# Performance work log

Measured on AMD Instinct MI355X. Metric: run time of the kernel, lower is better.

The kernel has to match this reference:

```python
import jax, jax.numpy as jnp
import numpy as np

B, N, CZ, CH, CA, H, TN = 1, 256, 128, 128, 32, 4, 4


def setup_inputs() -> dict:
    key = jax.random.key(0)
    ks = iter(jax.random.split(key, 64))

    def rn(shape, s=0.02):
        return jax.random.normal(next(ks), shape, dtype=jnp.float32) * s

    d = {"z": jax.random.normal(next(ks), (B, N, N, CZ), dtype=jnp.float32)}
    # Triangle multiplication params, stacked [2, ...]: idx 0 = outgoing, 1 = incoming
    d["tm_ln_in_w"] = jnp.ones((2, CZ)); d["tm_ln_in_b"] = jnp.zeros((2, CZ))
    for nm, shp in [("ap", (2, CZ, CH)), ("ag", (2, CZ, CH)), ("bp", (2, CZ, CH)),
                    ("bg", (2, CZ, CH)), ("g", (2, CZ, CZ)), ("zo", (2, CH, CZ))]:
        d[f"tm_{nm}_w"] = rn(shp)
        d[f"tm_{nm}_b"] = jnp.zeros((2, shp[-1]))
    d["tm_lnout_w"] = jnp.ones((2, CH)); d["tm_lnout_b"] = jnp.zeros((2, CH))
    # Triangle attention params, stacked [2, ...]: idx 0 = start, 1 = end
    d["ta_ln_w"] = jnp.ones((2, CZ)); d["ta_ln_b"] = jnp.zeros((2, CZ))
    d["ta_q_w"] = rn((2, CZ, H * CA)); d["ta_k_w"] = rn((2, CZ, H * CA)); d["ta_v_w"] = rn((2, CZ, H * CA))
    d["ta_b_w"] = rn((2, CZ, H))
    d["ta_g_w"] = rn((2, CZ, H * CA)); d["ta_g_b"] = jnp.zeros((2, H * CA))
    d["ta_o_w"] = rn((2, H * CA, CZ)); d["ta_o_b"] = jnp.zeros((2, CZ))
    # Pair transition
    d["pt_ln_w"] = jnp.ones((CZ,)); d["pt_ln_b"] = jnp.zeros((CZ,))
    d["pt_1_w"] = rn((CZ, TN * CZ)); d["pt_1_b"] = jnp.zeros((TN * CZ,))
    d["pt_2_w"] = rn((TN * CZ, CZ)); d["pt_2_b"] = jnp.zeros((CZ,))
    return d


def _ln(x, w, b, eps=1e-5):
    m = jnp.mean(x, axis=-1, keepdims=True)
    v = jnp.mean(jnp.square(x - m), axis=-1, keepdims=True)
    return (x - m) * jax.lax.rsqrt(v + eps) * w + b


def _tri_mul(z, lnw, lnb, apw, apb, agw, agb, bpw, bpb, bgw, bgb, gw, gb,
             lnow, lnob, zw, zb, outgoing):
    x = _ln(z, lnw, lnb)
    a = jax.nn.sigmoid(x @ agw + agb) * (x @ apw + apb)  # [B,I,J,CH]
    b = jax.nn.sigmoid(x @ bgw + bgb) * (x @ bpw + bpb)
    eq = 'bikc,bjkc->bijc' if outgoing else 'bkic,bkjc->bijc'
    t = jnp.einsum(eq, a, b)  # O(N^3 * CH)
    t = _ln(t, lnow, lnob) @ zw + zb
    return t * jax.nn.sigmoid(x @ gw + gb)


def _tri_att(z, lnw, lnb, qw, kw, vw, bw, gw, gb, ow, ob):
    Bz, I, J, _ = z.shape
    x = _ln(z, lnw, lnb)
    # triangle bias [B,1,H,I,J] (broadcast over query row)
    bias = jnp.einsum('bijc,ch->bhij', x, bw)[:, None]
    q = (x @ qw).reshape(Bz, I, J, H, CA).transpose(0, 1, 3, 2, 4) / np.float32(np.sqrt(CA))
    k = (x @ kw).reshape(Bz, I, J, H, CA).transpose(0, 1, 3, 2, 4)
    v = (x @ vw).reshape(Bz, I, J, H, CA).transpose(0, 1, 3, 2, 4)
    a = jnp.einsum('bihqc,bihkc->bihqk', q, k) + bias  # [B,I,H,J,J]
    p = jax.nn.softmax(a, axis=-1)
    o = jnp.einsum('bihqk,bihkc->bihqc', p, v).transpose(0, 1, 3, 2, 4).reshape(Bz, I, J, H * CA)
    o = o * jax.nn.sigmoid(x @ gw + gb)
    return o @ ow + ob


def reference(z, tm_ln_in_w, tm_ln_in_b, tm_ap_w, tm_ap_b, tm_ag_w, tm_ag_b,
              tm_bp_w, tm_bp_b, tm_bg_w, tm_bg_b, tm_g_w, tm_g_b,
              tm_lnout_w, tm_lnout_b, tm_zo_w, tm_zo_b,
              ta_ln_w, ta_ln_b, ta_q_w, ta_k_w, ta_v_w, ta_b_w,
              ta_g_w, ta_g_b, ta_o_w, ta_o_b,
              pt_ln_w, pt_ln_b, pt_1_w, pt_1_b, pt_2_w, pt_2_b):
    def tm(zz, i, outgoing):
        return _tri_mul(zz, tm_ln_in_w[i], tm_ln_in_b[i], tm_ap_w[i], tm_ap_b[i],
                        tm_ag_w[i], tm_ag_b[i], tm_bp_w[i], tm_bp_b[i],
                        tm_bg_w[i], tm_bg_b[i], tm_g_w[i], tm_g_b[i],
                        tm_lnout_w[i], tm_lnout_b[i], tm_zo_w[i], tm_zo_b[i], outgoing)

    def ta(zz, i):
        return _tri_att(zz, ta_ln_w[i], ta_ln_b[i], ta_q_w[i], ta_k_w[i], ta_v_w[i],
                        ta_b_w[i], ta_g_w[i], ta_g_b[i], ta_o_w[i], ta_o_b[i])

    z = z + tm(z, 0, True)          # triangle mult outgoing + residual (dropout = eval identity)
    z = z + tm(z, 1, False)         # triangle mult incoming + residual
    z = z + ta(z, 0)                # triangle attention (starting node)
    zt = jnp.swapaxes(z, 1, 2)      # transpose for ending-node attention
    zt = zt + ta(zt, 1)
    z = jnp.swapaxes(zt, 1, 2)
    x = _ln(z, pt_ln_w, pt_ln_b)    # pair transition
    z = z + (jax.nn.relu(x @ pt_1_w + pt_1_b) @ pt_2_w + pt_2_b)
    return z
```

## Files before the change

kernel.cpp:

```cpp
#include <hip/hip_runtime.h>
#include <math.h>

#define N_  256
#define NN  65536
#define CZ  128
#define CH  128
#define H_  4
#define CA  32

typedef __attribute__((ext_vector_type(8))) short bf16x8;
typedef __attribute__((ext_vector_type(4))) float f32x4;

__device__ __forceinline__ float sigmoidf_(float x){ return 1.f/(1.f+__expf(-x)); }

__device__ __forceinline__ short f2b(float f){
  unsigned u = __float_as_uint(f);
  unsigned r = (u + 0x7fffu + ((u>>16)&1u)) >> 16;
  return (short)r;
}
__device__ __forceinline__ float b2f(short s){
  unsigned u = ((unsigned)(unsigned short)s) << 16;
  return __uint_as_float(u);
}
__device__ __forceinline__ unsigned pk_bf16(float lo, float hi){
  unsigned r;
  asm volatile("v_cvt_pk_bf16_f32 %0, %1, %2" : "=v"(r) : "v"(lo), "v"(hi));
  return r;
}

__device__ __forceinline__ void glds16(const void* g, const void* l){
  __builtin_amdgcn_global_load_lds((const __attribute__((address_space(1))) void*)g,
                                   (__attribute__((address_space(3))) void*)l, 16, 0, 0);
}

__device__ __forceinline__ float wave_red_sum(float v){
  #pragma unroll
  for(int o=32;o>0;o>>=1) v += __shfl_xor(v,o,64);
  return v;
}

__device__ __forceinline__ int Gperm(int t, int m){
  return ((t>>1)<<5) + ((m>>2)<<3) + ((t&1)<<2) + (m&3);
}

__global__ void __launch_bounds__(256) prep_weights(
    const float* tm_ag, const float* tm_ap, const float* tm_bg, const float* tm_bp,
    const float* tm_g, const float* tm_zo,
    const float* ta_q, const float* ta_k, const float* ta_v, const float* ta_g, const float* ta_o,
    const float* pt1, const float* pt2, short* Wf){
  int tid = threadIdx.x;
  int g = blockIdx.x*4 + (tid>>6);
  int l = tid & 63;
  int s = blockIdx.y;
  const float* src; int ldn = 128, koff = 0, noff = 0;
  if (s < 12){
    int i = s/6, w = s - i*6;
    switch(w){ case 0: src=tm_ag; break; case 1: src=tm_ap; break; case 2: src=tm_bg; break;
               case 3: src=tm_bp; break; case 4: src=tm_g;  break; default: src=tm_zo; }
    src += i*16384;
  } else if (s < 22){
    int t2 = s-12; int i = t2/5, w = t2 - i*5;
    switch(w){ case 0: src=ta_q; break; case 1: src=ta_k; break; case 2: src=ta_v; break;
               case 3: src=ta_g; break; default: src=ta_o; }
    src += i*16384;
  } else if (s < 26){
    src = pt1; ldn = 512; noff = (s-22)*128;
  } else {
    src = pt2; koff = (s-26)*128;
  }
  int nt = g>>2, ks = g&3;
  int n = noff + nt*16 + (l&15);
  int kb = koff + ks*32 + (l>>4)*8;
  short tmp[8];
  #pragma unroll
  for (int e=0;e<8;e++) tmp[e] = f2b(src[(size_t)(kb+e)*ldn + n]);
  short* dst = Wf + s*16384 + ((nt*4+ks)*64 + l)*8;
  *(short4*)dst     = *(short4*)&tmp[0];
  *(short4*)(dst+4) = *(short4*)&tmp[4];
}

template<bool TRANS>
__global__ void __launch_bounds__(256) ln_x(const float* __restrict__ in,
                                            const float* __restrict__ w,
                                            const float* __restrict__ b,
                                            short* __restrict__ out){
  int wid  = threadIdx.x >> 6;
  int lane = threadIdx.x & 63;
  int row  = blockIdx.x*4 + wid;
  int irow;
  if (TRANS){ int i = row >> 8, j = row & 255; irow = (j<<8) | i; } else irow = row;
  float v0 = in[(size_t)irow*CZ + lane];
  float v1 = in[(size_t)irow*CZ + lane + 64];
  float m  = wave_red_sum(v0+v1) * (1.f/128.f);
  float d0 = v0-m, d1 = v1-m;
  float var = wave_red_sum(d0*d0 + d1*d1) * (1.f/128.f);
  float r = rsqrtf(var + 1e-5f);
  out[(size_t)row*CZ + lane]      = f2b(d0*r*w[lane]    + b[lane]);
  out[(size_t)row*CZ + lane + 64] = f2b(d1*r*w[lane+64] + b[lane+64]);
}

__device__ __forceinline__ void stage128_8(const short* __restrict__ g, short* xs, int r0, int tid){
  #pragma unroll
  for (int m=0;m<4;++m){
    int d = m*512 + tid;
    int row = d>>4, cw = d&15;
    glds16(&g[(size_t)(r0+row)*128 + ((cw ^ (row&15))<<3)], xs + (size_t)(d & ~63)*8);
  }
}

__device__ __forceinline__ bf16x8 ldsA(const short* xs, int row, int ch){
  return *(const bf16x8*)&xs[row*128 + ((ch ^ (row&15))<<3)];
}

__device__ __forceinline__ void gemm_core8(const short* xs, const short* __restrict__ wf,
                                           int wm, int wn, int l, f32x4 (&acc)[2][4]){
  #pragma unroll
  for (int ks=0; ks<4; ++ks){
    bf16x8 a[2], b[4];
    #pragma unroll
    for (int mt=0; mt<2; ++mt)
      a[mt] = ldsA(xs, wm*32 + mt*16 + (l&15), ks*4 + (l>>4));
    #pragma unroll
    for (int nt=0; nt<4; ++nt)
      b[nt] = *(const bf16x8*)&wf[(((wn*4+nt)*4 + ks)*64 + l)*8];
    #pragma unroll
    for (int mt=0; mt<2; ++mt)
      #pragma unroll
      for (int nt=0; nt<4; ++nt)
        acc[mt][nt] = __builtin_amdgcn_mfma_f32_16x16x32_bf16(a[mt], b[nt], acc[mt][nt], 0,0,0);
  }
}

__device__ __forceinline__ void gemm_core28(const short* xs, const short* __restrict__ wf1,
                                            const short* __restrict__ wf2,
                                            int wm, int wn, int l,
                                            f32x4 (&acc1)[2][4], f32x4 (&acc2)[2][4]){
  #pragma unroll
  for (int ks=0; ks<4; ++ks){
    bf16x8 a[2], b1[4], b2[4];
    #pragma unroll
    for (int mt=0; mt<2; ++mt)
      a[mt] = ldsA(xs, wm*32 + mt*16 + (l&15), ks*4 + (l>>4));
    #pragma unroll
    for (int nt=0; nt<4; ++nt){
      b1[nt] = *(const bf16x8*)&wf1[(((wn*4+nt)*4 + ks)*64 + l)*8];
      b2[nt] = *(const bf16x8*)&wf2[(((wn*4+nt)*4 + ks)*64 + l)*8];
    }
    #pragma unroll
    for (int mt=0; mt<2; ++mt)
      #pragma unroll
      for (int nt=0; nt<4; ++nt){
        acc1[mt][nt] = __builtin_amdgcn_mfma_f32_16x16x32_bf16(a[mt], b1[nt], acc1[mt][nt], 0,0,0);
        acc2[mt][nt] = __builtin_amdgcn_mfma_f32_16x16x32_bf16(a[mt], b2[nt], acc2[mt][nt], 0,0,0);
      }
  }
}

#define ZERO_ACC(A) { _Pragma("unroll") for(int _a=0;_a<2;_a++) _Pragma("unroll") for(int _b=0;_b<4;_b++) A[_a][_b]=(f32x4){0,0,0,0}; }

#define GEMM_PROLOG8 \
  int tid = threadIdx.x; int r0 = blockIdx.x*128; \
  int wid = tid>>6, l = tid&63; int wm = wid>>1, wn = wid&1; (void)r0;

#define EPI8 \
  int row = wm*32 + mt*16 + ((l>>4)<<2) + reg; \
  int col = wn*64 + nt*16 + (l&15);

#define FOR_EPI for (int mt=0;mt<2;++mt) for (int nt=0;nt<4;++nt) for (int reg=0;reg<4;++reg)

__global__ void __launch_bounds__(512) k_quad_gate(const short* __restrict__ X,
                                                   const short* __restrict__ Wagf, const float* __restrict__ bag,
                                                   const short* __restrict__ Wapf, const float* __restrict__ bap,
                                                   const short* __restrict__ Wbgf, const float* __restrict__ bbg,
                                                   const short* __restrict__ Wbpf, const float* __restrict__ bbp,
                                                   short* __restrict__ out1, short* __restrict__ out2){
  __shared__ short xs[128*128];
  GEMM_PROLOG8
  stage128_8(X, xs, r0, tid);
  __syncthreads();
  {
    f32x4 ag[2][4], ap[2][4];
    ZERO_ACC(ag) ZERO_ACC(ap)
    gemm_core28(xs, Wagf, Wapf, wm, wn, l, ag, ap);
    FOR_EPI{
      EPI8
      float v = (ap[mt][nt][reg] + bap[col]) * sigmoidf_(ag[mt][nt][reg] + bag[col]);
      out1[(size_t)(r0+row)*128 + col] = f2b(v);
    }
  }
  {
    f32x4 bg2[2][4], bp2[2][4];
    ZERO_ACC(bg2) ZERO_ACC(bp2)
    gemm_core28(xs, Wbgf, Wbpf, wm, wn, l, bg2, bp2);
    FOR_EPI{
      EPI8
      float v = (bp2[mt][nt][reg] + bbp[col]) * sigmoidf_(bg2[mt][nt][reg] + bbg[col]);
      out2[(size_t)(r0+row)*128 + col] = f2b(v);
    }
  }
}

__global__ void __launch_bounds__(512) k_qkv(const short* __restrict__ X,
                                             const short* __restrict__ Wqf, float sq,
                                             const short* __restrict__ Wkf,
                                             const short* __restrict__ Wvf,
                                             short* __restrict__ out_q, short* __restrict__ out_k,
                                             short* __restrict__ Vt){
  __shared__ short xs[128*128];
  GEMM_PROLOG8
  stage128_8(X, xs, r0, tid);
  __syncthreads();
  {
    f32x4 aq[2][4], ak[2][4];
    ZERO_ACC(aq) ZERO_ACC(ak)
    gemm_core28(xs, Wqf, Wkf, wm, wn, l, aq, ak);
    FOR_EPI{
      EPI8
      out_q[(size_t)(r0+row)*128 + col] = f2b(aq[mt][nt][reg]*sq);
      out_k[(size_t)(r0+row)*128 + col] = f2b(ak[mt][nt][reg]);
    }
  }
  f32x4 av[2][4];
  ZERO_ACC(av)
  gemm_core8(xs, Wvf, wm, wn, l, av);
  __syncthreads();
  #pragma unroll
  for (int mt=0;mt<2;++mt)
    #pragma unroll
    for (int nt=0;nt<4;++nt){
      int rb  = wm*32 + mt*16 + ((l>>4)<<2);
      int col = wn*64 + nt*16 + (l&15);
      short4 s4 = { f2b(av[mt][nt][0]), f2b(av[mt][nt][1]), f2b(av[mt][nt][2]), f2b(av[mt][nt][3]) };
      *(short4*)&xs[col*128 + (((rb>>3) ^ (col&15))<<3) + (rb&7)] = s4;
    }
  __syncthreads();
  int i = r0>>8, j0 = r0&255;
  #pragma unroll
  for (int m=0;m<4;++m){
    int d = m*512 + tid;
    int c = d>>4, ch = d&15;
    int4 val = *(const int4*)&xs[c*128 + ((ch ^ (c&15))<<3)];
    *(int4*)&Vt[(size_t)((i*4 + (c>>5))*32 + (c&31))*256 + j0 + ch*8] = val;
  }
}

__global__ void __launch_bounds__(512) k_tri_finish(const short* __restrict__ Tb,
                                                    const short* __restrict__ X,
                                                    const short* __restrict__ Wzf, const float* __restrict__ bz,
                                                    const short* __restrict__ Wgf, const float* __restrict__ bg,
                                                    const float* __restrict__ lnw, const float* __restrict__ lnb,
                                                    const float* __restrict__ zin, float* __restrict__ zout){
  __shared__ short tt[128*128];
  __shared__ short xs[128*128];
  __shared__ float ps[512], pq[512];
  __shared__ float mu[128], iv[128];
  GEMM_PROLOG8
  stage128_8(X, xs, r0, tid);
  #pragma unroll
  for (int m=0;m<4;++m){
    int d = m*512 + tid;
    int c = d>>4, ch = d&15;
    glds16(&Tb[(size_t)c*65536 + r0 + ch*8], tt + (size_t)(d & ~63)*8);
  }
  __syncthreads();
  int rl = tid & 127, cq = tid >> 7;
  float vals[32]; float s = 0.f, q = 0.f;
  #pragma unroll
  for (int cc=0; cc<32; ++cc){
    float v = b2f(tt[(cq*32+cc)*128 + rl]);
    vals[cc] = v; s += v; q += v*v;
  }
  ps[cq*128 + rl] = s; pq[cq*128 + rl] = q;
  __syncthreads();
  if (tid < 128){
    float ss = ps[tid]+ps[128+tid]+ps[256+tid]+ps[384+tid];
    float qq = pq[tid]+pq[128+tid]+pq[256+tid]+pq[384+tid];
    float m = ss * (1.f/128.f);
    float var = qq * (1.f/128.f) - m*m;
    mu[tid] = m; iv[tid] = rsqrtf(var + 1e-5f);
  }
  __syncthreads();
  {
    float m = mu[rl], r = iv[rl];
    #pragma unroll
    for (int chq=0; chq<4; ++chq){
      short tmp[8];
      #pragma unroll
      for (int e=0;e<8;++e){
        int cc = chq*8 + e;
        int c = cq*32 + cc;
        tmp[e] = f2b((vals[cc]-m)*r*lnw[c] + lnb[c]);
      }
      int ch = cq*4 + chq;
      *(int4*)&tt[rl*128 + ((ch ^ (rl&15))<<3)] = *(int4*)tmp;
    }
  }
  __syncthreads();
  f32x4 az[2][4], ag[2][4];
  ZERO_ACC(az) ZERO_ACC(ag)
  gemm_core8(tt, Wzf, wm, wn, l, az);
  gemm_core8(xs, Wgf, wm, wn, l, ag);
  FOR_EPI{
    EPI8
    size_t idx = (size_t)(r0+row)*128 + col;
    float v = (az[mt][nt][reg] + bz[col]) * sigmoidf_(ag[mt][nt][reg] + bg[col]);
    zout[idx] = zin[idx] + v;
  }
}

template<bool TRANS>
__global__ void __launch_bounds__(512) k_attn_out(const short* __restrict__ O,
                                                  const short* __restrict__ X,
                                                  const short* __restrict__ Wgf, const float* __restrict__ bg,
                                                  const short* __restrict__ Wof, const float* __restrict__ bo,
                                                  float* __restrict__ z){
  __shared__ short xs[128*128];
  __shared__ short os[128*128];
  GEMM_PROLOG8
  stage128_8(X, xs, r0, tid);
  #pragma unroll
  for (int m=0;m<4;++m){
    int d = m*512 + tid;
    int row = d>>4, ch = d&15;
    glds16(&O[(size_t)(r0+row)*128 + ch*8], os + (size_t)(d & ~63)*8);
  }
  __syncthreads();
  f32x4 ag[2][4];
  ZERO_ACC(ag)
  gemm_core8(xs, Wgf, wm, wn, l, ag);
  __syncthreads();
  FOR_EPI{
    EPI8
    float ov = b2f(os[row*128 + col]);
    float v = ov * sigmoidf_(ag[mt][nt][reg] + bg[col]);
    xs[row*128 + (((col>>3) ^ (row&15))<<3) + (col&7)] = f2b(v);
  }
  __syncthreads();
  f32x4 a2[2][4];
  ZERO_ACC(a2)
  gemm_core8(xs, Wof, wm, wn, l, a2);
  FOR_EPI{
    EPI8
    int orow = r0+row;
    int zrow = TRANS ? (((orow&255)<<8) | (orow>>8)) : orow;
    z[(size_t)zrow*128 + col] += a2[mt][nt][reg] + bo[col];
  }
}

__global__ void __launch_bounds__(512) k_pt(const short* __restrict__ X,
                                            const short* __restrict__ W1f, const float* __restrict__ b1,
                                            const short* __restrict__ W2f, const float* __restrict__ b2,
                                            float* __restrict__ z){
  __shared__ short xs[128*128];
  __shared__ short hs[128*128];
  GEMM_PROLOG8
  stage128_8(X, xs, r0, tid);
  __syncthreads();
  f32x4 a2[2][4];
  ZERO_ACC(a2)
  for (int m=0;m<4;++m){
    f32x4 a1[2][4];
    ZERO_ACC(a1)
    gemm_core8(xs, W1f + m*16384, wm, wn, l, a1);
    FOR_EPI{
      EPI8
      float v = fmaxf(a1[mt][nt][reg] + b1[m*128 + col], 0.f);
      hs[row*128 + (((col>>3) ^ (row&15))<<3) + (col&7)] = f2b(v);
    }
    __syncthreads();
    gemm_core8(hs, W2f + m*16384, wm, wn, l, a2);
    __syncthreads();
  }
  FOR_EPI{
    EPI8
    z[(size_t)(r0+row)*128 + col] += a2[mt][nt][reg] + b2[col];
  }
}

template<bool TR>
__global__ void __launch_bounds__(256) pack_cxy(const short* __restrict__ inA, const short* __restrict__ inB,
                                                short* __restrict__ outA, short* __restrict__ outB){
  __shared__ short tile[256*144];
  const short* in = blockIdx.y ? inB : inA;
  short* out      = blockIdx.y ? outB : outA;
  int x = blockIdx.x, tid = threadIdx.x;
  #pragma unroll
  for (int m=0;m<16;++m){
    int idx = m*256 + tid;
    int y = idx>>4, c0 = (idx&15)*8;
    int r = TR ? (y*256 + x) : (x*256 + y);
    *(int4*)&tile[y*144 + c0] = *(const int4*)&in[(size_t)r*128 + c0];
  }
  __syncthreads();
  int c = tid & 127, yh = tid >> 7;
  short* ob = out + (size_t)c*65536 + x*256 + yh*128;
  #pragma unroll
  for (int yc=0; yc<16; ++yc){
    short tmp[8];
    #pragma unroll
    for (int e=0;e<8;e++) tmp[e] = tile[(yh*128 + yc*8 + e)*144 + c];
    *(int4*)&ob[yc*8] = *(int4*)tmp;
  }
}

__global__ void __launch_bounds__(512) k_einsum(const short* __restrict__ Ab,
                                                const short* __restrict__ Bb,
                                                short* __restrict__ Tb){
  __shared__ short as[128*64];
  __shared__ short bs[128*64];
  int c = blockIdx.z;
  int i0 = blockIdx.x*128, j0 = blockIdx.y*128;
  const short* A = Ab + (size_t)c*65536;
  const short* B = Bb + (size_t)c*65536;
  int tid = threadIdx.x;
  int wid = tid>>6, l = tid&63; int wm = wid>>1, wn = wid&1;
  f32x4 acc[2][4];
  ZERO_ACC(acc)
  for (int kt=0; kt<4; ++kt){
    __syncthreads();
    #pragma unroll
    for (int m=0;m<2;++m){
      int d = m*512 + tid;
      int row = d>>3, cw = d&7;
      glds16(&A[(size_t)(i0+row)*256 + kt*64 + ((cw ^ (row&7))<<3)], as + (size_t)(d & ~63)*8);
      glds16(&B[(size_t)(j0+row)*256 + kt*64 + ((cw ^ (row&7))<<3)], bs + (size_t)(d & ~63)*8);
    }
    __syncthreads();
    #pragma unroll
    for (int ks=0; ks<2; ++ks){
      bf16x8 a[2], b[4];
      #pragma unroll
      for (int mt=0; mt<2; ++mt){
        int row = wm*32 + mt*16 + (l&15);
        int ch  = (ks*4 + (l>>4)) ^ (row&7);
        a[mt] = *(const bf16x8*)&as[row*64 + ch*8];
      }
      #pragma unroll
      for (int nt=0; nt<4; ++nt){
        int row = wn*64 + nt*16 + (l&15);
        int ch  = (ks*4 + (l>>4)) ^ (row&7);
        b[nt] = *(const bf16x8*)&bs[row*64 + ch*8];
      }
      #pragma unroll
      for (int mt=0; mt<2; ++mt)
        #pragma unroll
        for (int nt=0; nt<4; ++nt)
          acc[mt][nt] = __builtin_amdgcn_mfma_f32_16x16x32_bf16(a[mt], b[nt], acc[mt][nt], 0,0,0);
    }
  }
  short* To = Tb + (size_t)c*65536;
  FOR_EPI{
    int row = wm*32 + mt*16 + ((l>>4)<<2) + reg;
    int col = wn*64 + nt*16 + (l&15);
    To[(size_t)(i0+row)*256 + j0+col] = f2b(acc[mt][nt][reg]);
  }
}

__global__ void __launch_bounds__(256) bias_gemm(const short* __restrict__ X,
                                                 const float* __restrict__ bw,
                                                 float* __restrict__ BSF){
  __shared__ float xs[64][129];
  int r0 = blockIdx.x*64;
  for(int idx=threadIdx.x; idx<64*128; idx+=256)
    xs[idx>>7][idx&127] = b2f(X[(size_t)(r0+(idx>>7))*CZ + (idx&127)]);
  __syncthreads();
  int h = threadIdx.x>>6, r = threadIdx.x&63;
  float acc=0.f;
  #pragma unroll 4
  for(int k=0;k<CZ;k++) acc += xs[r][k]*bw[k*H_+h];
  int rr2 = r0 + r;
  int q = rr2 >> 8, j = rr2 & 255;
  int t = ((j>>5)<<1) + ((j>>2)&1);
  int m = (((j>>3)&3)<<2) + (j&3);
  int idx = (((h*16 + (q>>4))*16 + t) << 8) + (((m>>2)*16 + (q&15)) << 2) + (m&3);
  BSF[idx] = acc;
}

__global__ void __launch_bounds__(256, 3) attn_mfma(const short* __restrict__ Qg,
                                                    const short* __restrict__ Kg,
                                                    const short* __restrict__ Vt,
                                                    const float* __restrict__ BSF,
                                                    short* __restrict__ O){
  __shared__ short Kf[8192];
  __shared__ short Vf[8192];
  int i = blockIdx.x, h = blockIdx.y;
  int tid = threadIdx.x;
  #pragma unroll
  for (int m=0;m<4;++m){
    int d = m*256 + tid;
    int t = d>>6, ll = d&63;
    glds16(&Kg[(size_t)(i*N_ + Gperm(t, ll&15))*CH + h*CA + ((ll>>4)<<3)],
           Kf + (size_t)(d & ~63)*8);
    glds16(&Vt[(size_t)(((i*H_ + h)*CA) + ((t>>3)<<4) + (ll&15))*N_ + ((t&7)<<5) + ((ll>>4)<<3)],
           Vf + (size_t)(d & ~63)*8);
  }
  __syncthreads();

  int wid = tid >> 6, l = tid & 63;
  int lg = l >> 4, ln = l & 15;

  for (int ss=0; ss<4; ++ss){
    int sub = wid*4 + ss;
    bf16x8 qfrag = *(const bf16x8*)&Qg[(size_t)(i*N_ + sub*16 + ln)*CH + h*CA + (lg<<3)];
    const float* bb = BSF + (size_t)(h*16 + sub)*4096 + (l<<2);
    f32x4 acc[16];
    #pragma unroll
    for (int t=0;t<16;t++) acc[t] = *(const f32x4*)&bb[t<<8];
    #pragma unroll
    for (int t=0;t<16;t++){
      bf16x8 kf = *(const bf16x8*)&Kf[t*512 + l*8];
      acc[t] = __builtin_amdgcn_mfma_f32_16x16x32_bf16(kf, qfrag, acc[t], 0,0,0);
    }
    float mx = -1e30f;
    #pragma unroll
    for (int t=0;t<16;t++)
      mx = fmaxf(mx, fmaxf(fmaxf(acc[t][0],acc[t][1]), fmaxf(acc[t][2],acc[t][3])));
    mx = fmaxf(mx, __shfl_xor(mx,16,64));
    mx = fmaxf(mx, __shfl_xor(mx,32,64));
    float sum = 0.f;
    #pragma unroll
    for (int t=0;t<16;t++){
      #pragma unroll
      for (int r=0;r<4;r++){ float p = __expf(acc[t][r]-mx); acc[t][r]=p; sum += p; }
    }
    sum += __shfl_xor(sum,16,64);
    sum += __shfl_xor(sum,32,64);
    float iv = 1.0f / sum;
    bf16x8 pf[8];
    #pragma unroll
    for (int jt=0;jt<8;jt++){
      int4 w4;
      w4.x = pk_bf16(acc[2*jt  ][0], acc[2*jt  ][1]);
      w4.y = pk_bf16(acc[2*jt  ][2], acc[2*jt  ][3]);
      w4.z = pk_bf16(acc[2*jt+1][0], acc[2*jt+1][1]);
      w4.w = pk_bf16(acc[2*jt+1][2], acc[2*jt+1][3]);
      pf[jt] = *(bf16x8*)&w4;
    }
    #pragma unroll
    for (int ct=0; ct<2; ++ct){
      f32x4 oe = {0.f,0.f,0.f,0.f}, oo = {0.f,0.f,0.f,0.f};
      #pragma unroll
      for (int jt=0;jt<8;jt+=2){
        bf16x8 ve = *(const bf16x8*)&Vf[((ct*8 + jt  )*64 + l)*8];
        bf16x8 vo = *(const bf16x8*)&Vf[((ct*8 + jt+1)*64 + l)*8];
        oe = __builtin_amdgcn_mfma_f32_16x16x32_bf16(ve, pf[jt  ], oe, 0,0,0);
        oo = __builtin_amdgcn_mfma_f32_16x16x32_bf16(vo, pf[jt+1], oo, 0,0,0);
      }
      int q = sub*16 + ln;
      int c = ct*16 + lg*4;
      short4 ov = { f2b((oe[0]+oo[0])*iv), f2b((oe[1]+oo[1])*iv),
                    f2b((oe[2]+oo[2])*iv), f2b((oe[3]+oo[3])*iv) };
      *(short4*)&O[(size_t)(i*N_ + q)*CH + h*CA + c] = ov;
    }
  }
}

extern "C" void kernel_launch(void* const* d_in, const int* in_sizes, int n_in,
                              void* d_out, int out_size, void* d_ws, size_t ws_size,
                              hipStream_t stream) {
  const float* z_in      = (const float*)d_in[0];
  const float* tm_lnin_w = (const float*)d_in[1];
  const float* tm_lnin_b = (const float*)d_in[2];
  const float* tm_ap_w   = (const float*)d_in[3];
  const float* tm_ap_b   = (const float*)d_in[4];
  const float* tm_ag_w   = (const float*)d_in[5];
  const float* tm_ag_b   = (const float*)d_in[6];
  const float* tm_bp_w   = (const float*)d_in[7];
  const float* tm_bp_b   = (const float*)d_in[8];
  const float* tm_bg_w   = (const float*)d_in[9];
  const float* tm_bg_b   = (const float*)d_in[10];
  const float* tm_g_w    = (const float*)d_in[11];
  const float* tm_g_b    = (const float*)d_in[12];
  const float* tm_zo_w   = (const float*)d_in[13];
  const float* tm_zo_b   = (const float*)d_in[14];
  const float* tm_lno_w  = (const float*)d_in[15];
  const float* tm_lno_b  = (const float*)d_in[16];
  const float* ta_ln_w   = (const float*)d_in[17];
  const float* ta_ln_b   = (const float*)d_in[18];
  const float* ta_q_w    = (const float*)d_in[19];
  const float* ta_k_w    = (const float*)d_in[20];
  const float* ta_v_w    = (const float*)d_in[21];
  const float* ta_b_w    = (const float*)d_in[22];
  const float* ta_g_w    = (const float*)d_in[23];
  const float* ta_g_b    = (const float*)d_in[24];
  const float* ta_o_w    = (const float*)d_in[25];
  const float* ta_o_b    = (const float*)d_in[26];
  const float* pt_ln_w   = (const float*)d_in[27];
  const float* pt_ln_b   = (const float*)d_in[28];
  const float* pt_1_w    = (const float*)d_in[29];
  const float* pt_1_b    = (const float*)d_in[30];
  const float* pt_2_w    = (const float*)d_in[31];
  const float* pt_2_b    = (const float*)d_in[32];

  float* z  = (float*)d_out;
  char* base = (char*)d_ws;
  const size_t MB = 1u<<20;
  short* wf  = (short*)base;
  short* Xb  = (short*)(base + 1*MB);
  short* R1  = (short*)(base + 17*MB);
  short* R2  = (short*)(base + 33*MB);
  short* R3  = (short*)(base + 49*MB);
  short* R4  = (short*)(base + 65*MB);
  short* Tb  = (short*)(base + 81*MB);
  float* BSF = (float*)(base + 113*MB);

  #define SL(s) (wf + (size_t)(s)*16384)

  prep_weights<<<dim3(8,30), 256, 0, stream>>>(tm_ag_w, tm_ap_w, tm_bg_w, tm_bp_w,
                                               tm_g_w, tm_zo_w,
                                               ta_q_w, ta_k_w, ta_v_w, ta_g_w, ta_o_w,
                                               pt_1_w, pt_2_w, wf);

  for (int i=0;i<2;i++){
    const float* zsrc = (i==0) ? z_in : z;
    ln_x<false><<<NN/4, 256, 0, stream>>>(zsrc, tm_lnin_w+i*CZ, tm_lnin_b+i*CZ, Xb);
    k_quad_gate<<<NN/128, 512, 0, stream>>>(Xb, SL(i*6+0), tm_ag_b+i*CH, SL(i*6+1), tm_ap_b+i*CH,
                                            SL(i*6+2), tm_bg_b+i*CH, SL(i*6+3), tm_bp_b+i*CH,
                                            R1, R2);
    if (i==0) pack_cxy<false><<<dim3(256,2), 256, 0, stream>>>(R1, R2, R3, R4);
    else      pack_cxy<true ><<<dim3(256,2), 256, 0, stream>>>(R1, R2, R3, R4);
    k_einsum<<<dim3(2,2,128), 512, 0, stream>>>(R3, R4, Tb);
    k_tri_finish<<<NN/128, 512, 0, stream>>>(Tb, Xb, SL(i*6+5), tm_zo_b+i*CZ,
                                             SL(i*6+4), tm_g_b+i*CZ,
                                             tm_lno_w+i*CH, tm_lno_b+i*CH, zsrc, z);
  }

  for (int i=0;i<2;i++){
    if (i==0) ln_x<false><<<NN/4, 256, 0, stream>>>(z, ta_ln_w, ta_ln_b, Xb);
    else      ln_x<true ><<<NN/4, 256, 0, stream>>>(z, ta_ln_w+CZ, ta_ln_b+CZ, Xb);
    k_qkv<<<NN/128, 512, 0, stream>>>(Xb, SL(12+i*5+0), 0.17677669529663687f,
                                      SL(12+i*5+1), SL(12+i*5+2), R1, R2, R3);
    bias_gemm<<<NN/64, 256, 0, stream>>>(Xb, ta_b_w+i*CZ*H_, BSF);
    attn_mfma<<<dim3(N_,H_), 256, 0, stream>>>(R1, R2, R3, BSF, R4);
    if (i==0) k_attn_out<false><<<NN/128, 512, 0, stream>>>(R4, Xb, SL(12+i*5+3), ta_g_b+i*H_*CA,
                                                            SL(12+i*5+4), ta_o_b+i*CZ, z);
    else      k_attn_out<true ><<<NN/128, 512, 0, stream>>>(R4, Xb, SL(12+i*5+3), ta_g_b+i*H_*CA,
                                                            SL(12+i*5+4), ta_o_b+i*CZ, z);
  }

  ln_x<false><<<NN/4, 256, 0, stream>>>(z, pt_ln_w, pt_ln_b, Xb);
  k_pt<<<NN/128, 512, 0, stream>>>(Xb, SL(22), pt_1_b, SL(26), pt_2_b, z);
}
```

Baseline: 603.0 us.

## Fuse bias GEMM and pair LayerNorm, double-buffer einsum, restructure GEMM core

The triangle-attention bias projection moves into the QKV kernel, reusing its staged LDS tile, and the separate bias kernel is removed. The pair-transition LayerNorm is folded into k_pt, which drops one launch and one bf16 round trip through global memory. k_einsum double-buffers its A/B LDS tiles so the next k-slice loads while the current one is computed. The GEMM core is restructured to preload weight fragments in halves, and launch bounds are raised to 4 blocks per CU for occupancy, which may cause register spills.

Result: faster. 585.0 us (-3.0%).

```diff
diff --git a/kernel.cpp b/kernel.cpp
--- a/kernel.cpp
+++ b/kernel.cpp
@@ -112,47 +112,28 @@
   return *(const bf16x8*)&xs[row*128 + ((ch ^ (row&15))<<3)];
 }
 
-__device__ __forceinline__ void gemm_core8(const short* xs, const short* __restrict__ wf,
+__device__ __forceinline__ void gemm_coreP(const short* xs, const short* __restrict__ wf,
                                            int wm, int wn, int l, f32x4 (&acc)[2][4]){
   #pragma unroll
-  for (int ks=0; ks<4; ++ks){
-    bf16x8 a[2], b[4];
-    #pragma unroll
-    for (int mt=0; mt<2; ++mt)
-      a[mt] = ldsA(xs, wm*32 + mt*16 + (l&15), ks*4 + (l>>4));
-    #pragma unroll
-    for (int nt=0; nt<4; ++nt)
-      b[nt] = *(const bf16x8*)&wf[(((wn*4+nt)*4 + ks)*64 + l)*8];
-    #pragma unroll
-    for (int mt=0; mt<2; ++mt)
+  for (int kh=0; kh<2; ++kh){
+    bf16x8 b[2][4];
+    #pragma unroll
+    for (int ks2=0; ks2<2; ++ks2)
       #pragma unroll
       for (int nt=0; nt<4; ++nt)
-        acc[mt][nt] = __builtin_amdgcn_mfma_f32_16x16x32_bf16(a[mt], b[nt], acc[mt][nt], 0,0,0);
-  }
-}
-
-__device__ __forceinline__ void gemm_core28(const short* xs, const short* __restrict__ wf1,
-                                            const short* __restrict__ wf2,
-                                            int wm, int wn, int l,
-                                            f32x4 (&acc1)[2][4], f32x4 (&acc2)[2][4]){
-  #pragma unroll
-  for (int ks=0; ks<4; ++ks){
-    bf16x8 a[2], b1[4], b2[4];
-    #pragma unroll
-    for (int mt=0; mt<2; ++mt)
-      a[mt] = ldsA(xs, wm*32 + mt*16 + (l&15), ks*4 + (l>>4));
-    #pragma unroll
-    for (int nt=0; nt<4; ++nt){
-      b1[nt] = *(const bf16x8*)&wf1[(((wn*4+nt)*4 + ks)*64 + l)*8];
-      b2[nt] = *(const bf16x8*)&wf2[(((wn*4+nt)*4 + ks)*64 + l)*8];
-    }
-    #pragma unroll
-    for (int mt=0; mt<2; ++mt)
-      #pragma unroll
-      for (int nt=0; nt<4; ++nt){
-        acc1[mt][nt] = __builtin_amdgcn_mfma_f32_16x16x32_bf16(a[mt], b1[nt], acc1[mt][nt], 0,0,0);
-        acc2[mt][nt] = __builtin_amdgcn_mfma_f32_16x16x32_bf16(a[mt], b2[nt], acc2[mt][nt], 0,0,0);
-      }
+        b[ks2][nt] = *(const bf16x8*)&wf[(((wn*4+nt)*4 + kh*2+ks2)*64 + l)*8];
+    #pragma unroll
+    for (int ks2=0; ks2<2; ++ks2){
+      bf16x8 a[2];
+      #pragma unroll
+      for (int mt=0; mt<2; ++mt)
+        a[mt] = ldsA(xs, wm*32 + mt*16 + (l&15), (kh*2+ks2)*4 + (l>>4));
+      #pragma unroll
+      for (int mt=0; mt<2; ++mt)
+        #pragma unroll
+        for (int nt=0; nt<4; ++nt)
+          acc[mt][nt] = __builtin_amdgcn_mfma_f32_16x16x32_bf16(a[mt], b[ks2][nt], acc[mt][nt], 0,0,0);
+    }
   }
 }
 
@@ -168,12 +149,12 @@
 
 #define FOR_EPI for (int mt=0;mt<2;++mt) for (int nt=0;nt<4;++nt) for (int reg=0;reg<4;++reg)
 
-__global__ void __launch_bounds__(512) k_quad_gate(const short* __restrict__ X,
-                                                   const short* __restrict__ Wagf, const float* __restrict__ bag,
-                                                   const short* __restrict__ Wapf, const float* __restrict__ bap,
-                                                   const short* __restrict__ Wbgf, const float* __restrict__ bbg,
-                                                   const short* __restrict__ Wbpf, const float* __restrict__ bbp,
-                                                   short* __restrict__ out1, short* __restrict__ out2){
+__global__ void __launch_bounds__(512,4) k_quad_gate(const short* __restrict__ X,
+                                                     const short* __restrict__ Wagf, const float* __restrict__ bag,
+                                                     const short* __restrict__ Wapf, const float* __restrict__ bap,
+                                                     const short* __restrict__ Wbgf, const float* __restrict__ bbg,
+                                                     const short* __restrict__ Wbpf, const float* __restrict__ bbp,
+                                                     short* __restrict__ out1, short* __restrict__ out2){
   __shared__ short xs[128*128];
   GEMM_PROLOG8
   stage128_8(X, xs, r0, tid);
@@ -181,7 +162,8 @@
   {
     f32x4 ag[2][4], ap[2][4];
     ZERO_ACC(ag) ZERO_ACC(ap)
-    gemm_core28(xs, Wagf, Wapf, wm, wn, l, ag, ap);
+    gemm_coreP(xs, Wagf, wm, wn, l, ag);
+    gemm_coreP(xs, Wapf, wm, wn, l, ap);
     FOR_EPI{
       EPI8
       float v = (ap[mt][nt][reg] + bap[col]) * sigmoidf_(ag[mt][nt][reg] + bag[col]);
@@ -191,7 +173,8 @@
   {
     f32x4 bg2[2][4], bp2[2][4];
     ZERO_ACC(bg2) ZERO_ACC(bp2)
-    gemm_core28(xs, Wbgf, Wbpf, wm, wn, l, bg2, bp2);
+    gemm_coreP(xs, Wbgf, wm, wn, l, bg2);
+    gemm_coreP(xs, Wbpf, wm, wn, l, bp2);
     FOR_EPI{
       EPI8
       float v = (bp2[mt][nt][reg] + bbp[col]) * sigmoidf_(bg2[mt][nt][reg] + bbg[col]);
@@ -200,12 +183,13 @@
   }
 }
 
-__global__ void __launch_bounds__(512) k_qkv(const short* __restrict__ X,
-                                             const short* __restrict__ Wqf, float sq,
-                                             const short* __restrict__ Wkf,
-                                             const short* __restrict__ Wvf,
-                                             short* __restrict__ out_q, short* __restrict__ out_k,
-                                             short* __restrict__ Vt){
+__global__ void __launch_bounds__(512,4) k_qkv(const short* __restrict__ X,
+                                               const short* __restrict__ Wqf, float sq,
+                                               const short* __restrict__ Wkf,
+                                               const short* __restrict__ Wvf,
+                                               const float* __restrict__ bw,
+                                               short* __restrict__ out_q, short* __restrict__ out_k,
+                                               short* __restrict__ Vt, float* __restrict__ BSF){
   __shared__ short xs[128*128];
   GEMM_PROLOG8
   stage128_8(X, xs, r0, tid);
@@ -213,7 +197,8 @@
   {
     f32x4 aq[2][4], ak[2][4];
     ZERO_ACC(aq) ZERO_ACC(ak)
-    gemm_core28(xs, Wqf, Wkf, wm, wn, l, aq, ak);
+    gemm_coreP(xs, Wqf, wm, wn, l, aq);
+    gemm_coreP(xs, Wkf, wm, wn, l, ak);
     FOR_EPI{
       EPI8
       out_q[(size_t)(r0+row)*128 + col] = f2b(aq[mt][nt][reg]*sq);
@@ -222,7 +207,23 @@
   }
   f32x4 av[2][4];
   ZERO_ACC(av)
-  gemm_core8(xs, Wvf, wm, wn, l, av);
+  gemm_coreP(xs, Wvf, wm, wn, l, av);
+  {
+    int rl = tid & 127, hh = tid >> 7;
+    float bacc = 0.f;
+    #pragma unroll
+    for (int ch=0; ch<16; ++ch){
+      bf16x8 v = ldsA(xs, rl, ch);
+      #pragma unroll
+      for (int e=0;e<8;++e) bacc += b2f(v[e]) * bw[(ch*8+e)*H_ + hh];
+    }
+    int r = r0 + rl;
+    int qq = r >> 8, j = r & 255;
+    int t = ((j>>5)<<1) + ((j>>2)&1);
+    int mm = (((j>>3)&3)<<2) + (j&3);
+    int idx = (((hh*16 + (qq>>4))*16 + t) << 8) + (((mm>>2)*16 + (qq&15)) << 2) + (mm&3);
+    BSF[idx] = bacc;
+  }
   __syncthreads();
   #pragma unroll
   for (int mt=0;mt<2;++mt)
@@ -244,12 +245,12 @@
   }
 }
 
-__global__ void __launch_bounds__(512) k_tri_finish(const short* __restrict__ Tb,
-                                                    const short* __restrict__ X,
-                                                    const short* __restrict__ Wzf, const float* __restrict__ bz,
-                                                    const short* __restrict__ Wgf, const float* __restrict__ bg,
-                                                    const float* __restrict__ lnw, const float* __restrict__ lnb,
-                                                    const float* __restrict__ zin, float* __restrict__ zout){
+__global__ void __launch_bounds__(512,4) k_tri_finish(const short* __restrict__ Tb,
+                                                      const short* __restrict__ X,
+                                                      const short* __restrict__ Wzf, const float* __restrict__ bz,
+                                                      const short* __restrict__ Wgf, const float* __restrict__ bg,
+                                                      const float* __restrict__ lnw, const float* __restrict__ lnb,
+                                                      const float* __restrict__ zin, float* __restrict__ zout){
   __shared__ short tt[128*128];
   __shared__ short xs[128*128];
   __shared__ float ps[512], pq[512];
@@ -298,8 +299,8 @@
   __syncthreads();
   f32x4 az[2][4], ag[2][4];
   ZERO_ACC(az) ZERO_ACC(ag)
-  gemm_core8(tt, Wzf, wm, wn, l, az);
-  gemm_core8(xs, Wgf, wm, wn, l, ag);
+  gemm_coreP(tt, Wzf, wm, wn, l, az);
+  gemm_coreP(xs, Wgf, wm, wn, l, ag);
   FOR_EPI{
     EPI8
     size_t idx = (size_t)(r0+row)*128 + col;
@@ -309,11 +310,11 @@
 }
 
 template<bool TRANS>
-__global__ void __launch_bounds__(512) k_attn_out(const short* __restrict__ O,
-                                                  const short* __restrict__ X,
-                                                  const short* __restrict__ Wgf, const float* __restrict__ bg,
-                                                  const short* __restrict__ Wof, const float* __restrict__ bo,
-                                                  float* __restrict__ z){
+__global__ void __launch_bounds__(512,4) k_attn_out(const short* __restrict__ O,
+                                                    const short* __restrict__ X,
+                                                    const short* __restrict__ Wgf, const float* __restrict__ bg,
+                                                    const short* __restrict__ Wof, const float* __restrict__ bo,
+                                                    float* __restrict__ z){
   __shared__ short xs[128*128];
   __shared__ short os[128*128];
   GEMM_PROLOG8
@@ -327,7 +328,7 @@
   __syncthreads();
   f32x4 ag[2][4];
   ZERO_ACC(ag)
-  gemm_core8(xs, Wgf, wm, wn, l, ag);
+  gemm_coreP(xs, Wgf, wm, wn, l, ag);
   __syncthreads();
   FOR_EPI{
     EPI8
@@ -338,7 +339,7 @@
   __syncthreads();
   f32x4 a2[2][4];
   ZERO_ACC(a2)
-  gemm_core8(xs, Wof, wm, wn, l, a2);
+  gemm_coreP(xs, Wof, wm, wn, l, a2);
   FOR_EPI{
     EPI8
     int orow = r0+row;
@@ -347,28 +348,66 @@
   }
 }
 
-__global__ void __launch_bounds__(512) k_pt(const short* __restrict__ X,
-                                            const short* __restrict__ W1f, const float* __restrict__ b1,
-                                            const short* __restrict__ W2f, const float* __restrict__ b2,
-                                            float* __restrict__ z){
+__global__ void __launch_bounds__(512,4) k_pt(const float* __restrict__ lnw, const float* __restrict__ lnb,
+                                              const short* __restrict__ W1f, const float* __restrict__ b1,
+                                              const short* __restrict__ W2f, const float* __restrict__ b2,
+                                              float* __restrict__ z){
   __shared__ short xs[128*128];
   __shared__ short hs[128*128];
+  __shared__ float ps[512], pq[512];
+  __shared__ float mu[128], iv[128];
   GEMM_PROLOG8
-  stage128_8(X, xs, r0, tid);
+  int rl = tid & 127, cq = tid >> 7;
+  float vals[32]; float s = 0.f, q = 0.f;
+  {
+    const float* zr = &z[(size_t)(r0+rl)*128 + cq*32];
+    #pragma unroll
+    for (int cc=0; cc<32; cc+=4){
+      float4 v4 = *(const float4*)&zr[cc];
+      vals[cc]=v4.x; vals[cc+1]=v4.y; vals[cc+2]=v4.z; vals[cc+3]=v4.w;
+      s += v4.x+v4.y+v4.z+v4.w;
+      q += v4.x*v4.x + v4.y*v4.y + v4.z*v4.z + v4.w*v4.w;
+    }
+  }
+  ps[cq*128 + rl] = s; pq[cq*128 + rl] = q;
+  __syncthreads();
+  if (tid < 128){
+    float ss = ps[tid]+ps[128+tid]+ps[256+tid]+ps[384+tid];
+    float qq = pq[tid]+pq[128+tid]+pq[256+tid]+pq[384+tid];
+    float m = ss * (1.f/128.f);
+    float var = qq * (1.f/128.f) - m*m;
+    mu[tid] = m; iv[tid] = rsqrtf(var + 1e-5f);
+  }
+  __syncthreads();
+  {
+    float m = mu[rl], r = iv[rl];
+    #pragma unroll
+    for (int chq=0; chq<4; ++chq){
+      short tmp[8];
+      #pragma unroll
+      for (int e=0;e<8;++e){
+        int cc = chq*8 + e;
+        int c = cq*32 + cc;
+        tmp[e] = f2b((vals[cc]-m)*r*lnw[c] + lnb[c]);
+      }
+      int ch = cq*4 + chq;
+      *(int4*)&xs[rl*128 + ((ch ^ (rl&15))<<3)] = *(int4*)tmp;
+    }
+  }
   __syncthreads();
   f32x4 a2[2][4];
   ZERO_ACC(a2)
   for (int m=0;m<4;++m){
     f32x4 a1[2][4];
     ZERO_ACC(a1)
-    gemm_core8(xs, W1f + m*16384, wm, wn, l, a1);
+    gemm_coreP(xs, W1f + m*16384, wm, wn, l, a1);
     FOR_EPI{
       EPI8
       float v = fmaxf(a1[mt][nt][reg] + b1[m*128 + col], 0.f);
       hs[row*128 + (((col>>3) ^ (row&15))<<3) + (col&7)] = f2b(v);
     }
     __syncthreads();
-    gemm_core8(hs, W2f + m*16384, wm, wn, l, a2);
+    gemm_coreP(hs, W2f + m*16384, wm, wn, l, a2);
     __syncthreads();
   }
   FOR_EPI{
@@ -403,11 +442,11 @@
   }
 }
 
-__global__ void __launch_bounds__(512) k_einsum(const short* __restrict__ Ab,
-                                                const short* __restrict__ Bb,
-                                                short* __restrict__ Tb){
-  __shared__ short as[128*64];
-  __shared__ short bs[128*64];
+__global__ void __launch_bounds__(512,4) k_einsum(const short* __restrict__ Ab,
+                                                  const short* __restrict__ Bb,
+                                                  short* __restrict__ Tb){
+  __shared__ short as[2][128*64];
+  __shared__ short bs[2][128*64];
   int c = blockIdx.z;
   int i0 = blockIdx.x*128, j0 = blockIdx.y*128;
   const short* A = Ab + (size_t)c*65536;
@@ -416,16 +455,21 @@
   int wid = tid>>6, l = tid&63; int wm = wid>>1, wn = wid&1;
   f32x4 acc[2][4];
   ZERO_ACC(acc)
+
+  #define ESTAGE(buf, kt) { \
+    _Pragma("unroll") \
+    for (int m_=0;m_<2;++m_){ \
+      int d_ = m_*512 + tid; \
+      int row_ = d_>>3, cw_ = d_&7; \
+      glds16(&A[(size_t)(i0+row_)*256 + (kt)*64 + ((cw_ ^ (row_&7))<<3)], &as[buf][(d_ & ~63)*8]); \
+      glds16(&B[(size_t)(j0+row_)*256 + (kt)*64 + ((cw_ ^ (row_&7))<<3)], &bs[buf][(d_ & ~63)*8]); \
+    } }
+
+  ESTAGE(0, 0)
+  __syncthreads();
   for (int kt=0; kt<4; ++kt){
-    __syncthreads();
-    #pragma unroll
-    for (int m=0;m<2;++m){
-      int d = m*512 + tid;
-      int row = d>>3, cw = d&7;
-      glds16(&A[(size_t)(i0+row)*256 + kt*64 + ((cw ^ (row&7))<<3)], as + (size_t)(d & ~63)*8);
-      glds16(&B[(size_t)(j0+row)*256 + kt*64 + ((cw ^ (row&7))<<3)], bs + (size_t)(d & ~63)*8);
-    }
-    __syncthreads();
+    int cur = kt & 1;
+    if (kt < 3) ESTAGE(cur^1, kt+1)
     #pragma unroll
     for (int ks=0; ks<2; ++ks){
       bf16x8 a[2], b[4];
@@ -433,13 +477,13 @@
       for (int mt=0; mt<2; ++mt){
         int row = wm*32 + mt*16 + (l&15);
         int ch  = (ks*4 + (l>>4)) ^ (row&7);
-        a[mt] = *(const bf16x8*)&as[row*64 + ch*8];
+        a[mt] = *(const bf16x8*)&as[cur][row*64 + ch*8];
       }
       #pragma unroll
       for (int nt=0; nt<4; ++nt){
         int row = wn*64 + nt*16 + (l&15);
         int ch  = (ks*4 + (l>>4)) ^ (row&7);
-        b[nt] = *(const bf16x8*)&bs[row*64 + ch*8];
+        b[nt] = *(const bf16x8*)&bs[cur][row*64 + ch*8];
       }
       #pragma unroll
       for (int mt=0; mt<2; ++mt)
@@ -447,6 +491,7 @@
         for (int nt=0; nt<4; ++nt)
           acc[mt][nt] = __builtin_amdgcn_mfma_f32_16x16x32_bf16(a[mt], b[nt], acc[mt][nt], 0,0,0);
     }
+    __syncthreads();
   }
   short* To = Tb + (size_t)c*65536;
   FOR_EPI{
@@ -454,26 +499,6 @@
     int col = wn*64 + nt*16 + (l&15);
     To[(size_t)(i0+row)*256 + j0+col] = f2b(acc[mt][nt][reg]);
   }
-}
-
-__global__ void __launch_bounds__(256) bias_gemm(const short* __restrict__ X,
-                                                 const float* __restrict__ bw,
-                                                 float* __restrict__ BSF){
-  __shared__ float xs[64][129];
-  int r0 = blockIdx.x*64;
-  for(int idx=threadIdx.x; idx<64*128; idx+=256)
-    xs[idx>>7][idx&127] = b2f(X[(size_t)(r0+(idx>>7))*CZ + (idx&127)]);
-  __syncthreads();
-  int h = threadIdx.x>>6, r = threadIdx.x&63;
-  float acc=0.f;
-  #pragma unroll 4
-  for(int k=0;k<CZ;k++) acc += xs[r][k]*bw[k*H_+h];
-  int rr2 = r0 + r;
-  int q = rr2 >> 8, j = rr2 & 255;
-  int t = ((j>>5)<<1) + ((j>>2)&1);
-  int m = (((j>>3)&3)<<2) + (j&3);
-  int idx = (((h*16 + (q>>4))*16 + t) << 8) + (((m>>2)*16 + (q&15)) << 2) + (m&3);
-  BSF[idx] = acc;
 }
 
 __global__ void __launch_bounds__(256, 3) attn_mfma(const short* __restrict__ Qg,
@@ -629,8 +654,8 @@
     if (i==0) ln_x<false><<<NN/4, 256, 0, stream>>>(z, ta_ln_w, ta_ln_b, Xb);
     else      ln_x<true ><<<NN/4, 256, 0, stream>>>(z, ta_ln_w+CZ, ta_ln_b+CZ, Xb);
     k_qkv<<<NN/128, 512, 0, stream>>>(Xb, SL(12+i*5+0), 0.17677669529663687f,
-                                      SL(12+i*5+1), SL(12+i*5+2), R1, R2, R3);
-    bias_gemm<<<NN/64, 256, 0, stream>>>(Xb, ta_b_w+i*CZ*H_, BSF);
+                                      SL(12+i*5+1), SL(12+i*5+2), ta_b_w+i*CZ*H_,
+                                      R1, R2, R3, BSF);
     attn_mfma<<<dim3(N_,H_), 256, 0, stream>>>(R1, R2, R3, BSF, R4);
     if (i==0) k_attn_out<false><<<NN/128, 512, 0, stream>>>(R4, Xb, SL(12+i*5+3), ta_g_b+i*H_*CA,
                                                             SL(12+i*5+4), ta_o_b+i*CZ, z);
@@ -638,6 +663,5 @@
                                                             SL(12+i*5+4), ta_o_b+i*CZ, z);
   }
 
-  ln_x<false><<<NN/4, 256, 0, stream>>>(z, pt_ln_w, pt_ln_b, Xb);
-  k_pt<<<NN/128, 512, 0, stream>>>(Xb, SL(22), pt_1_b, SL(26), pt_2_b, z);
-}
+  k_pt<<<NN/128, 512, 0, stream>>>(pt_ln_w, pt_ln_b, SL(22), pt_1_b, SL(26), pt_2_b, z);
+}
```
